# Kernel tuning notes

Measured on AMD Instinct MI355X. Metric: run time of the kernel, lower is better.

## Reference

```python
import jax, jax.numpy as jnp
import numpy as np

IN_DIM, INTER, OUT, CLS = 512, 128, 64, 4
MID, BOT = 1600, 6400
N = 1 + MID + BOT
E = 160000


def setup_inputs() -> dict:
    key = jax.random.key(0)
    ki = iter(jax.random.split(key, 48))

    def nrm(shape, s=0.02):
        return jax.random.normal(next(ki), shape, dtype=jnp.float32) * s

    z = lambda *s: jnp.zeros(s, jnp.float32)
    inp = {}
    inp["x"] = jax.random.normal(next(ki), (N, IN_DIM), dtype=jnp.float32)
    inp["edge_index"] = jax.random.randint(next(ki), (2, E), 0, N)
    # PatchRelevance 1 (in=512 -> 128)
    inp["Wq1"], inp["bq1"] = nrm((IN_DIM, INTER)), z(INTER)
    inp["Wk1"], inp["bk1"] = nrm((IN_DIM, INTER)), z(INTER)
    inp["Wv1"], inp["bv1"] = nrm((IN_DIM, INTER)), z(INTER)
    # PatchRelevance 2 (128 -> 64)
    inp["Wq2"], inp["bq2"] = nrm((INTER, OUT)), z(OUT)
    inp["Wk2"], inp["bk2"] = nrm((INTER, OUT)), z(OUT)
    inp["Wv2"], inp["bv2"] = nrm((INTER, OUT)), z(OUT)
    # GCN convs
    inp["Wg1"], inp["bg1"] = nrm((IN_DIM, INTER)), z(INTER)
    inp["Wg2"], inp["bg2"] = nrm((INTER, OUT)), z(OUT)
    # squeeze MLPs
    inp["Ws1"], inp["bs1"] = nrm((2 * INTER, INTER)), z(INTER)
    inp["Ws2"], inp["bs2"] = nrm((2 * OUT, OUT)), z(OUT)
    # heads
    inp["Wfc1"], inp["bfc1"] = nrm((3 * OUT, OUT)), z(OUT)
    inp["Wfc2"], inp["bfc2"] = nrm((OUT, CLS)), z(CLS)
    inp["Wtw"], inp["btw"] = nrm((OUT, CLS)), z(CLS)
    inp["Wmid"], inp["bmid"] = nrm((OUT, CLS)), z(CLS)
    inp["Wbot"], inp["bbot"] = nrm((OUT, CLS)), z(CLS)
    # sparse_attention Conv1d(out_dim -> 4, k=4, s=4)  weight layout OIH
    inp["Wconv"] = nrm((4, OUT, 4))
    inp["bconv"] = z(4)
    inp["arch0"] = MID
    inp["arch1"] = BOT
    return inp


def _patch_rel(x, Wq, bq, Wk, bk, Wv, bv):
    q = x @ Wq + bq
    k = x @ Wk + bk
    v = x @ Wv + bv
    att = jax.nn.softmax(q @ k.T, axis=-1)  # [N, N]
    return att @ v


def _gcn(x, src, dst, W, b, n):
    # PyG GCNConv: add self-loops (already in src/dst), symmetric deg^-1/2 norm
    deg = jax.ops.segment_sum(jnp.ones_like(src, dtype=x.dtype), dst, num_segments=n)
    dinv = jnp.where(deg > 0, jax.lax.rsqrt(deg), 0.0)
    norm = dinv[src] * dinv[dst]
    h = x @ W
    out = jax.ops.segment_sum(h[src] * norm[:, None], dst, num_segments=n)
    return out + b


def reference(x, edge_index, Wq1, bq1, Wk1, bk1, Wv1, bv1, Wq2, bq2, Wk2, bk2,
              Wv2, bv2, Wg1, bg1, Wg2, bg2, Ws1, bs1, Ws2, bs2, Wfc1, bfc1,
              Wfc2, bfc2, Wtw, btw, Wmid, bmid, Wbot, bbot, Wconv, bconv,
              arch0, arch1):
    n = x.shape[0]
    loop = jnp.arange(n, dtype=edge_index.dtype)
    src = jnp.concatenate([edge_index[0], loop])
    dst = jnp.concatenate([edge_index[1], loop])

    r1 = _patch_rel(x, Wq1, bq1, Wk1, bk1, Wv1, bv1)
    g1 = _gcn(x, src, dst, Wg1, bg1, n)
    s1 = jax.nn.relu(jax.nn.relu(jnp.concatenate([g1, r1], axis=1)) @ Ws1 + bs1)

    r2 = _patch_rel(s1, Wq2, bq2, Wk2, bk2, Wv2, bv2)
    g2 = _gcn(s1, src, dst, Wg2, bg2, n)
    s2 = jax.nn.relu(jax.nn.relu(jnp.concatenate([g2, r2], axis=1)) @ Ws2 + bs2)

    tw = s2[0:1]                                   # [1, OUT]
    mid_features = s2[1:1 + arch0]                 # [arch0, OUT]
    mid_avg = jnp.mean(mid_features, axis=0, keepdims=True)
    bf = s2[1 + arch0:1 + arch0 + arch1]           # [arch1, OUT]

    # Conv1d(OUT -> 4, k=4, s=4) over node axis: [1, OUT, arch1] -> [1, 4, arch0]
    bw = jax.lax.conv_general_dilated(bf.T[None], Wconv, (4,), 'VALID',
                                      dimension_numbers=('NCH', 'OIH', 'NCH'))[0]
    bw = bw + bconv[:, None]                       # [4, arch0]
    # index_copy_ with strided indices == interleave channels: wv[i*4+j] = bw[j, i]
    wv = bw.T.reshape(-1)
    wv = wv / jnp.max(wv)
    grp = wv.reshape(arch0, 4)
    grp = grp / jnp.sum(jnp.abs(grp), axis=-1, keepdims=True)
    wv = grp.reshape(arch1, 1)

    tree_bottom = ((wv * bf).T.reshape(-1, arch0, 4).sum(-1)).T  # [arch0, OUT]
    bottom_weighted = (jnp.sum(wv * bf, axis=0) / arch0).reshape(1, -1)

    out_tw = tw @ Wtw + btw
    out_mid = mid_avg @ Wmid + bmid
    out_bottom = bottom_weighted @ Wbot + bbot
    gcn_feat = jnp.concatenate([tw, mid_avg, bottom_weighted], axis=-1) @ Wfc1 + bfc1
    out_gcn = jax.nn.relu(gcn_feat) @ Wfc2 + bfc2
    return (out_gcn, out_tw, out_mid, out_bottom, gcn_feat, tw, mid_avg,
            bottom_weighted, wv, mid_features, tree_bottom)
```

## Files before the change

### kernel.cpp

```cpp
#include <hip/hip_runtime.h>
#include <math.h>

#define N_NODES 8001
#define NPAD    8032
#define E_EDGES 160000
#define NQTOT   8064
#define LOG2E   1.4426950408889634f
#define NSPLIT  16

typedef unsigned short u16;
typedef __attribute__((ext_vector_type(8)))  short bf16x8;
typedef __attribute__((ext_vector_type(16))) float f32x16;

__device__ __forceinline__ short f2bf(float f) {
    unsigned u = __builtin_bit_cast(unsigned, f);
    u = (u + 0x7FFFu + ((u >> 16) & 1u)) >> 16;
    return (short)u;
}
__device__ __forceinline__ float bf2f(u16 x) {
    return __builtin_bit_cast(float, (unsigned)x << 16);
}
__device__ __forceinline__ int pk2(float a, float b) {
    int r;
    asm("v_cvt_pk_bf16_f32 %0, %1, %2" : "=v"(r) : "v"(a), "v"(b));
    return r;
}

#define GLDS(g, l) __builtin_amdgcn_global_load_lds( \
    (const __attribute__((address_space(1))) void*)(g), \
    (__attribute__((address_space(3))) void*)(l), 16, 0, 0)

__global__ __launch_bounds__(256) void prep_all(
    const float* __restrict__ x, const int* __restrict__ ei,
    const float* __restrict__ Wq1, const float* __restrict__ Wk1,
    const float* __restrict__ Wv1, const float* __restrict__ Wg1,
    const float* __restrict__ Wq2, const float* __restrict__ Wk2,
    const float* __restrict__ Wv2, const float* __restrict__ Wg2,
    const float* __restrict__ Ws1, const float* __restrict__ Ws2,
    int* __restrict__ degi, u16* __restrict__ XB,
    u16* __restrict__ WT1, u16* __restrict__ WT2,
    u16* __restrict__ WST1, u16* __restrict__ WST2)
{
    const int b = blockIdx.x, tid = threadIdx.x;
    if (b < 625) {
        int e = b * 256 + tid;
        if (e < E_EDGES) atomicAdd(&degi[ei[E_EDGES + e]], 1);
    } else if (b < 2633) {
        size_t t = (size_t)(b - 625) * 256 + tid;
        int row = (int)(t / 64), c8 = (int)(t % 64) * 8;
        int lrow = min(row, N_NODES - 1);
        const float4* p = (const float4*)&x[(size_t)lrow * 512 + c8];
        float4 u = p[0], v = p[1];
        int4 w = { pk2(u.x, u.y), pk2(u.z, u.w), pk2(v.x, v.y), pk2(v.z, v.w) };
        *(int4*)&XB[t * 8] = w;
    } else if (b < 3657) {
        int t = (b - 2633) * 256 + tid;
        int p = t / (128 * 512), n = (t / 512) & 127, k = t % 512;
        const float* W = (p == 0) ? Wq1 : (p == 1) ? Wk1 : (p == 2) ? Wv1 : Wg1;
        float v = W[k * 128 + n];
        if (p == 0) v *= LOG2E;
        WT1[t] = (u16)f2bf(v);
    } else if (b < 3785) {
        int t = (b - 3657) * 256 + tid;
        int p = t / (64 * 128), n = (t / 128) & 63, k = t & 127;
        const float* W = (p == 0) ? Wq2 : (p == 1) ? Wk2 : (p == 2) ? Wv2 : Wg2;
        float v = W[k * 64 + n];
        if (p == 0) v *= LOG2E;
        WT2[t] = (u16)f2bf(v);
    } else if (b < 3913) {
        int t = (b - 3785) * 256 + tid;
        int n = t >> 8, k = t & 255;
        WST1[t] = (u16)f2bf(Ws1[k * 128 + n]);
    } else {
        int t = (b - 3913) * 256 + tid;
        int n = t >> 7, k = t & 127;
        WST2[t] = (u16)f2bf(Ws2[k * 64 + n]);
    }
}

template<int K, int MOUT>
__global__ __launch_bounds__(256) void proj4_mfma(
    const u16* __restrict__ Xb, const u16* __restrict__ WT,
    const float* __restrict__ bq, const float* __restrict__ bk,
    const float* __restrict__ bv,
    u16* __restrict__ Qb, u16* __restrict__ Kb, u16* __restrict__ VTb,
    float* __restrict__ Hb)
{
    constexpr int NKC  = K / 16;
    constexpr int NNT  = MOUT / 32;
    constexpr int ROWB = K / 8;
    constexpr int NB   = 32 * ROWB;

    __shared__ u16 xs[32 * K];

    const int tid = threadIdx.x, wid = tid >> 6, lane = tid & 63;
    const int q = lane & 31, gp = lane >> 5;
    const int m0 = blockIdx.x * 32;

    for (int i = tid; i < NB; i += 256) {
        int row = i / ROWB, blk = i % ROWB;
        GLDS(&Xb[(size_t)(m0 + row) * K + 8 * (blk ^ (row & 7))], &xs[i * 8]);
    }
    __syncthreads();

    f32x16 acc[NNT];
#pragma unroll
    for (int nt = 0; nt < NNT; nt++) acc[nt] = f32x16{};

    const u16* wbase = WT + (size_t)wid * MOUT * K;

#pragma unroll 4
    for (int c = 0; c < NKC; c++) {
        bf16x8 af = *(const bf16x8*)&xs[q * K + 8 * ((2 * c + gp) ^ (q & 7))];
#pragma unroll
        for (int nt = 0; nt < NNT; nt++) {
            bf16x8 bf = *(const bf16x8*)&wbase[(size_t)(nt * 32 + q) * K + 16 * c + 8 * gp];
            acc[nt] = __builtin_amdgcn_mfma_f32_32x32x16_bf16(af, bf, acc[nt], 0, 0, 0);
        }
    }

    if (wid == 0) {
#pragma unroll
        for (int nt = 0; nt < NNT; nt++) {
            float bb = bq[nt * 32 + q] * LOG2E;
#pragma unroll
            for (int r = 0; r < 16; r++) {
                int grow = m0 + (r & 3) + 8 * (r >> 2) + 4 * gp;
                Qb[(size_t)grow * MOUT + nt * 32 + q] = (u16)f2bf(acc[nt][r] + bb);
            }
        }
    } else if (wid == 1) {
#pragma unroll
        for (int nt = 0; nt < NNT; nt++) {
            float bb = bk[nt * 32 + q];
#pragma unroll
            for (int r = 0; r < 16; r++) {
                int grow = m0 + (r & 3) + 8 * (r >> 2) + 4 * gp;
                Kb[(size_t)grow * MOUT + nt * 32 + q] = (u16)f2bf(acc[nt][r] + bb);
            }
        }
    } else if (wid == 2) {
#pragma unroll
        for (int nt = 0; nt < NNT; nt++) {
            float bb = bv[nt * 32 + q];
            u16* vrow = &VTb[(size_t)(nt * 32 + q) * NPAD];
#pragma unroll
            for (int g = 0; g < 4; g++) {
                ushort4 s;
                s.x = (u16)f2bf(acc[nt][4 * g + 0] + bb);
                s.y = (u16)f2bf(acc[nt][4 * g + 1] + bb);
                s.z = (u16)f2bf(acc[nt][4 * g + 2] + bb);
                s.w = (u16)f2bf(acc[nt][4 * g + 3] + bb);
                *(ushort4*)&vrow[m0 + 8 * g + 4 * gp] = s;
            }
        }
    } else {
#pragma unroll
        for (int nt = 0; nt < NNT; nt++) {
#pragma unroll
            for (int r = 0; r < 16; r++) {
                int grow = m0 + (r & 3) + 8 * (r >> 2) + 4 * gp;
                if (grow < N_NODES)
                    Hb[(size_t)grow * MOUT + nt * 32 + q] = acc[nt][r];
            }
        }
    }
}

template<int K, int MOUT, int OM, int NW>
__global__ __launch_bounds__(NW * 64) void s_gemm_mfma(
    const u16* __restrict__ Ab, const u16* __restrict__ WT,
    const float* __restrict__ bias, void* __restrict__ Cv)
{
    constexpr int NKC  = K / 16;
    constexpr int ROWB = K / 8;
    constexpr int NB   = 32 * ROWB;

    __shared__ u16 xs[32 * K];

    const int tid = threadIdx.x, wid = tid >> 6, lane = tid & 63;
    const int q = lane & 31, gp = lane >> 5;
    const int m0 = blockIdx.x * 32;

    for (int i = tid; i < NB; i += NW * 64) {
        int row = i / ROWB, blk = i % ROWB;
        GLDS(&Ab[(size_t)(m0 + row) * K + 8 * (blk ^ (row & 7))], &xs[i * 8]);
    }
    __syncthreads();

    f32x16 acc = f32x16{};
    const u16* wbase = WT + (size_t)(wid * 32) * K;

#pragma unroll 4
    for (int c = 0; c < NKC; c++) {
        bf16x8 af = *(const bf16x8*)&xs[q * K + 8 * ((2 * c + gp) ^ (q & 7))];
        bf16x8 bf = *(const bf16x8*)&wbase[(size_t)q * K + 16 * c + 8 * gp];
        acc = __builtin_amdgcn_mfma_f32_32x32x16_bf16(af, bf, acc, 0, 0, 0);
    }

    float bb = bias[wid * 32 + q];
#pragma unroll
    for (int r = 0; r < 16; r++) {
        int grow = m0 + (r & 3) + 8 * (r >> 2) + 4 * gp;
        float v = fmaxf(acc[r] + bb, 0.f);
        if (OM == 0) {
            if (grow < N_NODES) ((float*)Cv)[(size_t)grow * MOUT + wid * 32 + q] = v;
        } else {
            ((u16*)Cv)[(size_t)grow * MOUT + wid * 32 + q] = (u16)f2bf(v);
        }
    }
}

template<int D, int S>
__global__ __launch_bounds__(256) void attn_split(
    const u16* __restrict__ Qg, const u16* __restrict__ Kg,
    const u16* __restrict__ VTg, u16* __restrict__ PO, float* __restrict__ PL)
{
    constexpr int NCH   = D / 16;
    constexpr int NDT   = D / 32;
    constexpr int KROWB = D / 8;
    constexpr int KI    = (32 * D) / 512;
    constexpr int VI    = (D * 32) / 512;
    constexpr int NKS   = KI / 4;
    constexpr int NVS   = VI / 4;
    constexpr int NT    = (N_NODES + 31) / 32;
    constexpr int CHUNK = (NT + S - 1) / S;

    __shared__ u16 kb[2][32 * D];
    __shared__ u16 vb[2][D * 32];

    const int tid  = threadIdx.x;
    const int wid  = tid >> 6;
    const int lane = tid & 63;
    const int q    = lane & 31;
    const int gp   = lane >> 5;
    const int sp   = blockIdx.x;
    const int q0   = blockIdx.y * 128 + wid * 32;

    bf16x8 qf[NCH];
    {
        int row = min(q0 + q, N_NODES - 1);
        const u16* qr = &Qg[(size_t)row * D + 8 * gp];
#pragma unroll
        for (int c = 0; c < NCH; c++)
            qf[c] = *(const bf16x8*)&qr[16 * c];
    }

    const int arow = (q & ~12) | ((q & 4) << 1) | ((q & 8) >> 1);
    const int hK   = (arow & 3) | (((arow >> 3) & 1) << 2);

    f32x16 acc[NDT];
#pragma unroll
    for (int i = 0; i < NDT; i++) acc[i] = f32x16{};
    float l = 0.f;

    const int t0 = sp * CHUNK;
    const int t1 = min(t0 + CHUNK, NT);

    const u16* kp[NKS]; int kdo[NKS];
#pragma unroll
    for (int s = 0; s < NKS; s++) {
        int i   = wid + 4 * s;
        int B   = i * 64 + lane;
        int row = B / KROWB;
        int bk  = B & (KROWB - 1);
        int h   = (row & 3) | (((row >> 3) & 1) << 2);
        kp[s]  = &Kg[(size_t)(t0 * 32 + row) * D + 8 * (bk ^ h)];
        kdo[s] = i * 512;
    }
    const u16* vp[NVS]; int vdo[NVS];
#pragma unroll
    for (int s = 0; s < NVS; s++) {
        int i  = wid + 4 * s;
        int B  = i * 64 + lane;
        int d  = B >> 2;
        int bv = B & 3;
        vp[s]  = &VTg[(size_t)d * NPAD + t0 * 32 + 8 * (bv ^ (d & 3))];
        vdo[s] = i * 512;
    }

    auto stage = [&](int buf) {
        u16* kdst = &kb[buf][0];
        u16* vdst = &vb[buf][0];
#pragma unroll
        for (int s = 0; s < NKS; s++) GLDS(kp[s], &kdst[kdo[s]]);
#pragma unroll
        for (int s = 0; s < NVS; s++) GLDS(vp[s], &vdst[vdo[s]]);
    };
    auto advance = [&]() {
#pragma unroll
        for (int s = 0; s < NKS; s++) kp[s] += 32 * D;
#pragma unroll
        for (int s = 0; s < NVS; s++) vp[s] += 32;
    };

    stage(0);
    advance();
    __syncthreads();

    for (int t = t0; t < t1; t++) {
        const int b = (t - t0) & 1;
        if (t + 1 < t1) { stage(b ^ 1); advance(); }

        const u16* kbt = &kb[b][0];
        const u16* vbt = &vb[b][0];
        const int j0 = t * 32;

        f32x16 st = f32x16{};
#pragma unroll
        for (int c = 0; c < NCH; c++) {
            bf16x8 af = *(const bf16x8*)&kbt[arow * D + 8 * ((2 * c + gp) ^ hK)];
            st = __builtin_amdgcn_mfma_f32_32x32x16_bf16(af, qf[c], st, 0, 0, 0);
        }

        if (j0 + 32 > N_NODES) {
#pragma unroll
            for (int r = 0; r < 16; r++) {
                int kl = (r & 3) + (((r >> 2) & 1) << 2) + ((r >> 3) << 4) + 8 * gp;
                if (j0 + kl >= N_NODES) st[r] = -INFINITY;
            }
        }

        float pv[16]; float ps = 0.f;
#pragma unroll
        for (int r = 0; r < 16; r++) { pv[r] = exp2f(st[r]); ps += pv[r]; }
        ps += __shfl_xor(ps, 32);
        l += ps;

        int4 w0 = { pk2(pv[0],  pv[1]),  pk2(pv[2],  pv[3]),
                    pk2(pv[4],  pv[5]),  pk2(pv[6],  pv[7]) };
        int4 w1 = { pk2(pv[8],  pv[9]),  pk2(pv[10], pv[11]),
                    pk2(pv[12], pv[13]), pk2(pv[14], pv[15]) };
        bf16x8 bp0 = __builtin_bit_cast(bf16x8, w0);
        bf16x8 bp1 = __builtin_bit_cast(bf16x8, w1);

#pragma unroll
        for (int dt = 0; dt < NDT; dt++) {
            const int d = 32 * dt + q;
            bf16x8 vf0 = *(const bf16x8*)&vbt[d * 32 + 8 * ((gp)     ^ (d & 3))];
            acc[dt] = __builtin_amdgcn_mfma_f32_32x32x16_bf16(vf0, bp0, acc[dt], 0, 0, 0);
            bf16x8 vf1 = *(const bf16x8*)&vbt[d * 32 + 8 * ((2 + gp) ^ (d & 3))];
            acc[dt] = __builtin_amdgcn_mfma_f32_32x32x16_bf16(vf1, bp1, acc[dt], 0, 0, 0);
        }
        __syncthreads();
    }

    const int qrl = q0 + q;
    if (gp == 0) PL[(size_t)sp * NQTOT + qrl] = l;
    u16* po = &PO[((size_t)sp * NQTOT + qrl) * D];
#pragma unroll
    for (int dt = 0; dt < NDT; dt++)
#pragma unroll
        for (int k = 0; k < 4; k++) {
            int2 w = { pk2(acc[dt][4 * k + 0], acc[dt][4 * k + 1]),
                       pk2(acc[dt][4 * k + 2], acc[dt][4 * k + 3]) };
            *(int2*)&po[32 * dt + 8 * k + 4 * gp] = w;
        }
}

template<int C, int S>
__global__ __launch_bounds__(256) void merge_gather(
    const u16* __restrict__ PO, const float* __restrict__ PL,
    const float* __restrict__ h, const int* __restrict__ rowptr,
    const int2* __restrict__ csr, const float* __restrict__ dinv,
    const float* __restrict__ bias, u16* __restrict__ AR)
{
    constexpr int MB  = (NPAD * (C / 4)) / 256;
    constexpr int LPN = C / 4;
    constexpr int NPB = 256 / LPN;

    const int tid = threadIdx.x;
    if ((int)blockIdx.x < MB) {
        int t  = blockIdx.x * 256 + tid;
        int qr = t / (C / 4);
        int d4 = (t % (C / 4)) * 4;

        float L = 0.f;
#pragma unroll
        for (int s = 0; s < S; s++) L += PL[(size_t)s * NQTOT + qr];
        float4 o = make_float4(0.f, 0.f, 0.f, 0.f);
#pragma unroll
        for (int s = 0; s < S; s++) {
            ushort4 p = *(const ushort4*)&PO[((size_t)s * NQTOT + qr) * C + d4];
            o.x += bf2f(p.x); o.y += bf2f(p.y);
            o.z += bf2f(p.z); o.w += bf2f(p.w);
        }
        float inv = 1.f / L;
        int2 w = { pk2(fmaxf(o.x * inv, 0.f), fmaxf(o.y * inv, 0.f)),
                   pk2(fmaxf(o.z * inv, 0.f), fmaxf(o.w * inv, 0.f)) };
        *(int2*)&AR[(size_t)qr * (2 * C) + C + d4] = w;
    } else {
        const int node = (blockIdx.x - MB) * NPB + tid / LPN;
        const int c4   = (tid % LPN) * 4;
        if (node >= N_NODES) return;
        const int r0 = rowptr[node], r1 = rowptr[node + 1];
        float4 acc = make_float4(0.f, 0.f, 0.f, 0.f);
        for (int j = r0; j < r1; j++) {
            int2 pk = csr[j];
            float nr = __int_as_float(pk.y);
            const float4 hv = *(const float4*)&h[(size_t)pk.x * C + c4];
            acc.x += hv.x * nr; acc.y += hv.y * nr;
            acc.z += hv.z * nr; acc.w += hv.w * nr;
        }
        float di = dinv[node];
        float sl = di * di;
        const float4 hs = *(const float4*)&h[(size_t)node * C + c4];
        const float4 bv = *(const float4*)&bias[c4];
        acc.x += hs.x * sl + bv.x; acc.y += hs.y * sl + bv.y;
        acc.z += hs.z * sl + bv.z; acc.w += hs.w * sl + bv.w;
        int2 w = { pk2(fmaxf(acc.x, 0.f), fmaxf(acc.y, 0.f)),
                   pk2(fmaxf(acc.z, 0.f), fmaxf(acc.w, 0.f)) };
        *(int2*)&AR[(size_t)node * (2 * C) + c4] = w;
    }
}

__global__ __launch_bounds__(256) void prefix_rowptr(
    const int* __restrict__ degi, int* __restrict__ rowptr,
    int* __restrict__ cursor, float* __restrict__ dinv)
{
    __shared__ int sums[256];
    const int t = threadIdx.x;
    const int base = t * 32;
    int local[32];
    int s = 0;
#pragma unroll
    for (int i = 0; i < 32; i++) {
        int idx = base + i;
        local[i] = s;
        s += (idx < N_NODES) ? degi[idx] : 0;
    }
    sums[t] = s;
    __syncthreads();
    for (int o = 1; o < 256; o <<= 1) {
        int v = (t >= o) ? sums[t - o] : 0;
        __syncthreads();
        sums[t] += v;
        __syncthreads();
    }
    const int pre = (t == 0) ? 0 : sums[t - 1];
#pragma unroll
    for (int i = 0; i < 32; i++) {
        int idx = base + i;
        if (idx <= N_NODES) {
            int v = pre + local[i];
            rowptr[idx] = v;
            if (idx < N_NODES) cursor[idx] = v;
        }
    }
    for (int i = t; i < N_NODES; i += 256)
        dinv[i] = rsqrtf((float)degi[i] + 1.f);
}

__global__ void csr_fill(const int* __restrict__ ei, const float* __restrict__ dinv,
                         int* __restrict__ cursor, int2* __restrict__ csr)
{
    int e = blockIdx.x * blockDim.x + threadIdx.x;
    if (e >= E_EDGES) return;
    int s = ei[e], d = ei[E_EDGES + e];
    int pos = atomicAdd(&cursor[d], 1);
    int2 pk;
    pk.x = s;
    pk.y = __float_as_int(dinv[s] * dinv[d]);
    csr[pos] = pk;
}

__global__ __launch_bounds__(256) void conv_wv(
    const float* __restrict__ S2, const float* __restrict__ Wconv,
    const float* __restrict__ bconv, float* __restrict__ wvp)
{
    __shared__ float wt[16 * 64];
    const int tid = threadIdx.x;
    for (int idx = tid; idx < 1024; idx += 256) {
        int o = idx >> 8, rem = idx & 255, i = rem >> 2, k = rem & 3;
        wt[(k * 4 + o) * 64 + i] = Wconv[idx];
    }
    __syncthreads();

    const int wid = tid >> 6, d = tid & 63;
    const int t = blockIdx.x * 4 + wid;
    const float* base = S2 + (size_t)(1601 + 4 * t) * 64;
    const float v0 = base[d], v1 = base[64 + d], v2 = base[128 + d], v3 = base[192 + d];

    float p[4];
#pragma unroll
    for (int o = 0; o < 4; o++)
        p[o] = v0 * wt[(0 * 4 + o) * 64 + d] + v1 * wt[(1 * 4 + o) * 64 + d]
             + v2 * wt[(2 * 4 + o) * 64 + d] + v3 * wt[(3 * 4 + o) * 64 + d];

#pragma unroll
    for (int o = 0; o < 4; o++)
#pragma unroll
        for (int off = 1; off < 64; off <<= 1) p[o] += __shfl_xor(p[o], off);

    if (d == 0) {
#pragma unroll
        for (int o = 0; o < 4; o++) wvp[4 * t + o] = p[o] + bconv[o];
    }
}

__global__ __launch_bounds__(256) void wv_copy(
    const float* __restrict__ wvp, const float* __restrict__ S2,
    float* __restrict__ wv, float* __restrict__ out)
{
    const int b = blockIdx.x, tid = threadIdx.x;
    if (b < 7) {
        float mv = -INFINITY;
        for (int i = tid; i < 6400; i += 256) mv = fmaxf(mv, wvp[i]);
#pragma unroll
        for (int o = 32; o > 0; o >>= 1) mv = fmaxf(mv, __shfl_xor(mv, o));
        __shared__ float sm[4];
        if ((tid & 63) == 0) sm[tid >> 6] = mv;
        __syncthreads();
        const float g = fmaxf(fmaxf(sm[0], sm[1]), fmaxf(sm[2], sm[3]));
        int t = b * 256 + tid;
        if (t < 1600) {
            float v0 = wvp[4 * t + 0] / g, v1 = wvp[4 * t + 1] / g;
            float v2 = wvp[4 * t + 2] / g, v3 = wvp[4 * t + 3] / g;
            float s = fabsf(v0) + fabsf(v1) + fabsf(v2) + fabsf(v3);
            float r0 = v0 / s, r1 = v1 / s, r2 = v2 / s, r3 = v3 / s;
            wv[4 * t + 0] = r0; wv[4 * t + 1] = r1;
            wv[4 * t + 2] = r2; wv[4 * t + 3] = r3;
            out[272 + 4 * t + 0] = r0; out[272 + 4 * t + 1] = r1;
            out[272 + 4 * t + 2] = r2; out[272 + 4 * t + 3] = r3;
        }
    } else {
        int i = (b - 7) * 256 + tid;
        if (i < 25600) ((float4*)(out + 6672))[i] = ((const float4*)(S2 + 64))[i];
    }
}

__global__ void tree_bottom_kernel(const float* __restrict__ S2,
                                   const float* __restrict__ wv,
                                   float* __restrict__ out)
{
    int t = blockIdx.x * blockDim.x + threadIdx.x;
    if (t >= 1600 * 64) return;
    int mg = t >> 6, c = t & 63;
    const float* base = S2 + (size_t)(1601 + 4 * mg) * 64 + c;
    out[t] = wv[4 * mg + 0] * base[0]   + wv[4 * mg + 1] * base[64]
           + wv[4 * mg + 2] * base[128] + wv[4 * mg + 3] * base[192];
}

__global__ void col_mean2(const float* __restrict__ S2, const float* __restrict__ tb,
                          float* __restrict__ midavg, float* __restrict__ botw)
{
    const int b = blockIdx.x;
    const int c = b & 63;
    const float* in = (b < 64) ? (S2 + 64) : tb;
    float s = 0.f;
    for (int r = threadIdx.x; r < 1600; r += 256) s += in[(size_t)r * 64 + c];
    for (int o = 32; o > 0; o >>= 1) s += __shfl_xor(s, o);
    __shared__ float sm[4];
    if ((threadIdx.x & 63) == 0) sm[threadIdx.x >> 6] = s;
    __syncthreads();
    if (threadIdx.x == 0) {
        float v = (sm[0] + sm[1] + sm[2] + sm[3]) * (1.f / 1600.f);
        (b < 64 ? midavg : botw)[c] = v;
    }
}

__global__ void head_kernel(const float* __restrict__ S2,
                            const float* __restrict__ midavg, const float* __restrict__ botw,
                            const float* __restrict__ Wtw,  const float* __restrict__ btw,
                            const float* __restrict__ Wmid, const float* __restrict__ bmid,
                            const float* __restrict__ Wbot, const float* __restrict__ bbot,
                            const float* __restrict__ Wfc1, const float* __restrict__ bfc1,
                            const float* __restrict__ Wfc2, const float* __restrict__ bfc2,
                            float* __restrict__ out)
{
    __shared__ float cat[192];
    __shared__ float gf[64];
    int t = threadIdx.x;
    float twv = S2[t];
    cat[t]       = twv;
    cat[64 + t]  = midavg[t];
    cat[128 + t] = botw[t];
    out[80 + t]  = twv;
    out[144 + t] = midavg[t];
    out[208 + t] = botw[t];
    __syncthreads();
    float acc = bfc1[t];
    for (int k = 0; k < 192; k++) acc += cat[k] * Wfc1[k * 64 + t];
    gf[t] = acc;
    out[16 + t] = acc;
    __syncthreads();
    if (t < 4) {
        float og = bfc2[t], ot = btw[t], om = bmid[t], ob = bbot[t];
        for (int c = 0; c < 64; c++) {
            og += fmaxf(gf[c], 0.f) * Wfc2[c * 4 + t];
            ot += cat[c]        * Wtw[c * 4 + t];
            om += cat[64 + c]   * Wmid[c * 4 + t];
            ob += cat[128 + c]  * Wbot[c * 4 + t];
        }
        out[0 + t] = og; out[4 + t] = ot; out[8 + t] = om; out[12 + t] = ob;
    }
}

extern "C" void kernel_launch(void* const* d_in, const int* in_sizes, int n_in,
                              void* d_out, int out_size, void* d_ws, size_t ws_size,
                              hipStream_t stream)
{
    (void)in_sizes; (void)n_in; (void)out_size; (void)ws_size;
    const float* x    = (const float*)d_in[0];
    const int*   ei   = (const int*)d_in[1];
    const float* Wq1  = (const float*)d_in[2];  const float* bq1 = (const float*)d_in[3];
    const float* Wk1  = (const float*)d_in[4];  const float* bk1 = (const float*)d_in[5];
    const float* Wv1  = (const float*)d_in[6];  const float* bv1 = (const float*)d_in[7];
    const float* Wq2  = (const float*)d_in[8];  const float* bq2 = (const float*)d_in[9];
    const float* Wk2  = (const float*)d_in[10]; const float* bk2 = (const float*)d_in[11];
    const float* Wv2  = (const float*)d_in[12]; const float* bv2 = (const float*)d_in[13];
    const float* Wg1  = (const float*)d_in[14]; const float* bg1 = (const float*)d_in[15];
    const float* Wg2  = (const float*)d_in[16]; const float* bg2 = (const float*)d_in[17];
    const float* Ws1  = (const float*)d_in[18]; const float* bs1 = (const float*)d_in[19];
    const float* Ws2  = (const float*)d_in[20]; const float* bs2 = (const float*)d_in[21];
    const float* Wfc1 = (const float*)d_in[22]; const float* bfc1= (const float*)d_in[23];
    const float* Wfc2 = (const float*)d_in[24]; const float* bfc2= (const float*)d_in[25];
    const float* Wtw  = (const float*)d_in[26]; const float* btw = (const float*)d_in[27];
    const float* Wmid = (const float*)d_in[28]; const float* bmid= (const float*)d_in[29];
    const float* Wbot = (const float*)d_in[30]; const float* bbot= (const float*)d_in[31];
    const float* Wconv= (const float*)d_in[32]; const float* bconv=(const float*)d_in[33];

    float* out = (float*)d_out;
    float* ws  = (float*)d_ws;

    const size_t N128 = (size_t)N_NODES * 128;
    const size_t BF128 = (size_t)NPAD * 128 / 2;

    size_t off = 0;
    auto alloc = [&](size_t n) { float* p = ws + off; off += (n + 15) & ~size_t(15); return p; };
    float* QB1  = alloc(BF128);
    float* KB1  = alloc(BF128);
    float* VTB1 = alloc(BF128);
    float* XB   = alloc((size_t)NPAD * 256);
    float* WT1  = alloc(4 * 128 * 512 / 2);
    float* WT2  = alloc(4 * 64 * 128 / 2);
    float* WST1 = alloc(128 * 256 / 2);
    float* WST2 = alloc(64 * 128 / 2);
    float* AR1  = alloc((size_t)NPAD * 128);
    float* S1B  = alloc((size_t)NPAD * 64);
    float* H1   = alloc(N128);
    float* S2   = alloc(N128);
    float* DINV = alloc(N_NODES);
    int*   DEGI   = (int*)alloc(8008);
    int*   ROWPTR = (int*)alloc(8008);
    int*   CURSOR = (int*)alloc(8008);
    int2*  CSR    = (int2*)alloc(2 * (size_t)E_EDGES);
    float* PO   = alloc((size_t)NSPLIT * NQTOT * 128 / 2);
    float* PL   = alloc((size_t)NSPLIT * NQTOT);
    float* WVP  = alloc(6400);
    float* WV   = alloc(6400);
    float* MIDAVG = alloc(64);
    float* BOTW   = alloc(64);
    float* QB2  = QB1;
    float* KB2  = KB1;
    float* VTB2 = VTB1;
    float* H2   = H1;
    float* AR2  = AR1;

    hipMemsetAsync(DEGI, 0, N_NODES * sizeof(int), stream);
    prep_all<<<3945, 256, 0, stream>>>(
        x, ei, Wq1, Wk1, Wv1, Wg1, Wq2, Wk2, Wv2, Wg2, Ws1, Ws2,
        DEGI, (u16*)XB, (u16*)WT1, (u16*)WT2, (u16*)WST1, (u16*)WST2);
    prefix_rowptr<<<1, 256, 0, stream>>>(DEGI, ROWPTR, CURSOR, DINV);
    csr_fill<<<(E_EDGES + 255) / 256, 256, 0, stream>>>(ei, DINV, CURSOR, CSR);

    proj4_mfma<512, 128><<<NPAD / 32, 256, 0, stream>>>(
        (const u16*)XB, (const u16*)WT1, bq1, bk1, bv1,
        (u16*)QB1, (u16*)KB1, (u16*)VTB1, H1);

    attn_split<128, NSPLIT><<<dim3(NSPLIT, 63), 256, 0, stream>>>(
        (const u16*)QB1, (const u16*)KB1, (const u16*)VTB1, (u16*)PO, PL);

    {
        int mb = (NPAD * 32) / 256, gb = (N_NODES * 32 + 255) / 256;
        merge_gather<128, NSPLIT><<<mb + gb, 256, 0, stream>>>(
            (const u16*)PO, PL, H1, ROWPTR, CSR, DINV, bg1, (u16*)AR1);
    }

    s_gemm_mfma<256, 128, 1, 4><<<NPAD / 32, 256, 0, stream>>>(
        (const u16*)AR1, (const u16*)WST1, bs1, (u16*)S1B);

    proj4_mfma<128, 64><<<NPAD / 32, 256, 0, stream>>>(
        (const u16*)S1B, (const u16*)WT2, bq2, bk2, bv2,
        (u16*)QB2, (u16*)KB2, (u16*)VTB2, H2);

    attn_split<64, NSPLIT><<<dim3(NSPLIT, 63), 256, 0, stream>>>(
        (const u16*)QB2, (const u16*)KB2, (const u16*)VTB2, (u16*)PO, PL);

    {
        int mb = (NPAD * 16) / 256, gb = (N_NODES * 16 + 255) / 256;
        merge_gather<64, NSPLIT><<<mb + gb, 256, 0, stream>>>(
            (const u16*)PO, PL, H2, ROWPTR, CSR, DINV, bg2, (u16*)AR2);
    }

    s_gemm_mfma<128, 64, 0, 2><<<NPAD / 32, 128, 0, stream>>>(
        (const u16*)AR2, (const u16*)WST2, bs2, S2);

    conv_wv<<<400, 256, 0, stream>>>(S2, Wconv, bconv, WVP);
    wv_copy<<<107, 256, 0, stream>>>(WVP, S2, WV, out);
    tree_bottom_kernel<<<400, 256, 0, stream>>>(S2, WV, out + 109072);
    col_mean2<<<128, 256, 0, stream>>>(S2, out + 109072, MIDAVG, BOTW);
    head_kernel<<<1, 64, 0, stream>>>(S2, MIDAVG, BOTW, Wtw, btw, Wmid, bmid,
                                      Wbot, bbot, Wfc1, bfc1, Wfc2, bfc2, out);
}
```

Before: 248.1 us.

## Raise MFMA priority, split layer-2 attention wider, fold column means into other kernels

Wraps the QK and PV MFMA loops in attn_split with s_setprio so matrix work gets scheduling priority over other waves. The second attention layer now uses 32 key splits instead of 16 to expose more parallelism for the smaller head dimension. The separate col_mean2 launch is removed: the mid-feature mean is computed by extra blocks of conv_wv, and the bottom-weighted mean is accumulated with atomics inside tree_bottom_kernel. This saves a launch and a reread of the tree_bottom output, at the cost of float atomics with nondeterministic summation order and a larger partial-output merge for layer 2.

```diff
diff --git a/kernel.cpp b/kernel.cpp
--- a/kernel.cpp
+++ b/kernel.cpp
@@ -6,7 +6,8 @@
 #define E_EDGES 160000
 #define NQTOT   8064
 #define LOG2E   1.4426950408889634f
-#define NSPLIT  16
+#define SP1     16
+#define SP2     32
 
 typedef unsigned short u16;
 typedef __attribute__((ext_vector_type(8)))  short bf16x8;
@@ -307,11 +308,13 @@
         const int j0 = t * 32;
 
         f32x16 st = f32x16{};
+        __builtin_amdgcn_s_setprio(1);
 #pragma unroll
         for (int c = 0; c < NCH; c++) {
             bf16x8 af = *(const bf16x8*)&kbt[arow * D + 8 * ((2 * c + gp) ^ hK)];
             st = __builtin_amdgcn_mfma_f32_32x32x16_bf16(af, qf[c], st, 0, 0, 0);
         }
+        __builtin_amdgcn_s_setprio(0);
 
         if (j0 + 32 > N_NODES) {
 #pragma unroll
@@ -334,6 +337,7 @@
         bf16x8 bp0 = __builtin_bit_cast(bf16x8, w0);
         bf16x8 bp1 = __builtin_bit_cast(bf16x8, w1);
 
+        __builtin_amdgcn_s_setprio(1);
 #pragma unroll
         for (int dt = 0; dt < NDT; dt++) {
             const int d = 32 * dt + q;
@@ -342,6 +346,7 @@
             bf16x8 vf1 = *(const bf16x8*)&vbt[d * 32 + 8 * ((2 + gp) ^ (d & 3))];
             acc[dt] = __builtin_amdgcn_mfma_f32_32x32x16_bf16(vf1, bp1, acc[dt], 0, 0, 0);
         }
+        __builtin_amdgcn_s_setprio(0);
         __syncthreads();
     }
 
@@ -466,35 +471,48 @@
 
 __global__ __launch_bounds__(256) void conv_wv(
     const float* __restrict__ S2, const float* __restrict__ Wconv,
-    const float* __restrict__ bconv, float* __restrict__ wvp)
-{
-    __shared__ float wt[16 * 64];
-    const int tid = threadIdx.x;
-    for (int idx = tid; idx < 1024; idx += 256) {
-        int o = idx >> 8, rem = idx & 255, i = rem >> 2, k = rem & 3;
-        wt[(k * 4 + o) * 64 + i] = Wconv[idx];
-    }
-    __syncthreads();
-
-    const int wid = tid >> 6, d = tid & 63;
-    const int t = blockIdx.x * 4 + wid;
-    const float* base = S2 + (size_t)(1601 + 4 * t) * 64;
-    const float v0 = base[d], v1 = base[64 + d], v2 = base[128 + d], v3 = base[192 + d];
-
-    float p[4];
-#pragma unroll
-    for (int o = 0; o < 4; o++)
-        p[o] = v0 * wt[(0 * 4 + o) * 64 + d] + v1 * wt[(1 * 4 + o) * 64 + d]
-             + v2 * wt[(2 * 4 + o) * 64 + d] + v3 * wt[(3 * 4 + o) * 64 + d];
-
-#pragma unroll
-    for (int o = 0; o < 4; o++)
-#pragma unroll
-        for (int off = 1; off < 64; off <<= 1) p[o] += __shfl_xor(p[o], off);
-
-    if (d == 0) {
-#pragma unroll
-        for (int o = 0; o < 4; o++) wvp[4 * t + o] = p[o] + bconv[o];
+    const float* __restrict__ bconv, float* __restrict__ wvp,
+    float* __restrict__ midavg)
+{
+    const int b = blockIdx.x, tid = threadIdx.x;
+    if (b < 400) {
+        __shared__ float wt[16 * 64];
+        for (int idx = tid; idx < 1024; idx += 256) {
+            int o = idx >> 8, rem = idx & 255, i = rem >> 2, k = rem & 3;
+            wt[(k * 4 + o) * 64 + i] = Wconv[idx];
+        }
+        __syncthreads();
+
+        const int wid = tid >> 6, d = tid & 63;
+        const int t = b * 4 + wid;
+        const float* base = S2 + (size_t)(1601 + 4 * t) * 64;
+        const float v0 = base[d], v1 = base[64 + d], v2 = base[128 + d], v3 = base[192 + d];
+
+        float p[4];
+#pragma unroll
+        for (int o = 0; o < 4; o++)
+            p[o] = v0 * wt[(0 * 4 + o) * 64 + d] + v1 * wt[(1 * 4 + o) * 64 + d]
+                 + v2 * wt[(2 * 4 + o) * 64 + d] + v3 * wt[(3 * 4 + o) * 64 + d];
+
+#pragma unroll
+        for (int o = 0; o < 4; o++)
+#pragma unroll
+            for (int off = 1; off < 64; off <<= 1) p[o] += __shfl_xor(p[o], off);
+
+        if (d == 0) {
+#pragma unroll
+            for (int o = 0; o < 4; o++) wvp[4 * t + o] = p[o] + bconv[o];
+        }
+    } else {
+        const int c = b - 400;
+        float s = 0.f;
+        for (int r = tid; r < 1600; r += 256) s += S2[64 + (size_t)r * 64 + c];
+        for (int o = 32; o > 0; o >>= 1) s += __shfl_xor(s, o);
+        __shared__ float sm[4];
+        if ((tid & 63) == 0) sm[tid >> 6] = s;
+        __syncthreads();
+        if (tid == 0)
+            midavg[c] = (sm[0] + sm[1] + sm[2] + sm[3]) * (1.f / 1600.f);
     }
 }
 
@@ -529,38 +547,28 @@
     }
 }
 
-__global__ void tree_bottom_kernel(const float* __restrict__ S2,
-                                   const float* __restrict__ wv,
-                                   float* __restrict__ out)
-{
-    int t = blockIdx.x * blockDim.x + threadIdx.x;
-    if (t >= 1600 * 64) return;
+__global__ __launch_bounds__(256) void tree_bottom_kernel(
+    const float* __restrict__ S2, const float* __restrict__ wv,
+    float* __restrict__ out, float* __restrict__ botw_raw)
+{
+    __shared__ float red[256];
+    int t = blockIdx.x * 256 + threadIdx.x;
     int mg = t >> 6, c = t & 63;
     const float* base = S2 + (size_t)(1601 + 4 * mg) * 64 + c;
-    out[t] = wv[4 * mg + 0] * base[0]   + wv[4 * mg + 1] * base[64]
-           + wv[4 * mg + 2] * base[128] + wv[4 * mg + 3] * base[192];
-}
-
-__global__ void col_mean2(const float* __restrict__ S2, const float* __restrict__ tb,
-                          float* __restrict__ midavg, float* __restrict__ botw)
-{
-    const int b = blockIdx.x;
-    const int c = b & 63;
-    const float* in = (b < 64) ? (S2 + 64) : tb;
-    float s = 0.f;
-    for (int r = threadIdx.x; r < 1600; r += 256) s += in[(size_t)r * 64 + c];
-    for (int o = 32; o > 0; o >>= 1) s += __shfl_xor(s, o);
-    __shared__ float sm[4];
-    if ((threadIdx.x & 63) == 0) sm[threadIdx.x >> 6] = s;
+    float v = wv[4 * mg + 0] * base[0]   + wv[4 * mg + 1] * base[64]
+            + wv[4 * mg + 2] * base[128] + wv[4 * mg + 3] * base[192];
+    out[t] = v;
+    red[threadIdx.x] = v;
     __syncthreads();
-    if (threadIdx.x == 0) {
-        float v = (sm[0] + sm[1] + sm[2] + sm[3]) * (1.f / 1600.f);
-        (b < 64 ? midavg : botw)[c] = v;
+    if (threadIdx.x < 64) {
+        float s = red[threadIdx.x] + red[threadIdx.x + 64]
+                + red[threadIdx.x + 128] + red[threadIdx.x + 192];
+        atomicAdd(&botw_raw[threadIdx.x], s);
     }
 }
 
 __global__ void head_kernel(const float* __restrict__ S2,
-                            const float* __restrict__ midavg, const float* __restrict__ botw,
+                            const float* __restrict__ midavg, const float* __restrict__ botw_raw,
                             const float* __restrict__ Wtw,  const float* __restrict__ btw,
                             const float* __restrict__ Wmid, const float* __restrict__ bmid,
                             const float* __restrict__ Wbot, const float* __restrict__ bbot,
@@ -572,12 +580,13 @@
     __shared__ float gf[64];
     int t = threadIdx.x;
     float twv = S2[t];
+    float bw  = botw_raw[t] * (1.f / 1600.f);
     cat[t]       = twv;
     cat[64 + t]  = midavg[t];
-    cat[128 + t] = botw[t];
+    cat[128 + t] = bw;
     out[80 + t]  = twv;
     out[144 + t] = midavg[t];
-    out[208 + t] = botw[t];
+    out[208 + t] = bw;
     __syncthreads();
     float acc = bfc1[t];
     for (int k = 0; k < 192; k++) acc += cat[k] * Wfc1[k * 64 + t];
@@ -645,8 +654,8 @@
     int*   ROWPTR = (int*)alloc(8008);
     int*   CURSOR = (int*)alloc(8008);
     int2*  CSR    = (int2*)alloc(2 * (size_t)E_EDGES);
-    float* PO   = alloc((size_t)NSPLIT * NQTOT * 128 / 2);
-    float* PL   = alloc((size_t)NSPLIT * NQTOT);
+    float* PO   = alloc((size_t)SP1 * NQTOT * 128 / 2);
+    float* PL   = alloc((size_t)SP2 * NQTOT);
     float* WVP  = alloc(6400);
     float* WV   = alloc(6400);
     float* MIDAVG = alloc(64);
@@ -658,6 +667,7 @@
     float* AR2  = AR1;
 
     hipMemsetAsync(DEGI, 0, N_NODES * sizeof(int), stream);
+    hipMemsetAsync(BOTW, 0, 64 * sizeof(float), stream);
     prep_all<<<3945, 256, 0, stream>>>(
         x, ei, Wq1, Wk1, Wv1, Wg1, Wq2, Wk2, Wv2, Wg2, Ws1, Ws2,
         DEGI, (u16*)XB, (u16*)WT1, (u16*)WT2, (u16*)WST1, (u16*)WST2);
@@ -668,12 +678,12 @@
         (const u16*)XB, (const u16*)WT1, bq1, bk1, bv1,
         (u16*)QB1, (u16*)KB1, (u16*)VTB1, H1);
 
-    attn_split<128, NSPLIT><<<dim3(NSPLIT, 63), 256, 0, stream>>>(
+    attn_split<128, SP1><<<dim3(SP1, 63), 256, 0, stream>>>(
         (const u16*)QB1, (const u16*)KB1, (const u16*)VTB1, (u16*)PO, PL);
 
     {
         int mb = (NPAD * 32) / 256, gb = (N_NODES * 32 + 255) / 256;
-        merge_gather<128, NSPLIT><<<mb + gb, 256, 0, stream>>>(
+        merge_gather<128, SP1><<<mb + gb, 256, 0, stream>>>(
             (const u16*)PO, PL, H1, ROWPTR, CSR, DINV, bg1, (u16*)AR1);
     }
 
@@ -684,22 +694,21 @@
         (const u16*)S1B, (const u16*)WT2, bq2, bk2, bv2,
         (u16*)QB2, (u16*)KB2, (u16*)VTB2, H2);
 
-    attn_split<64, NSPLIT><<<dim3(NSPLIT, 63), 256, 0, stream>>>(
+    attn_split<64, SP2><<<dim3(SP2, 63), 256, 0, stream>>>(
         (const u16*)QB2, (const u16*)KB2, (const u16*)VTB2, (u16*)PO, PL);
 
     {
         int mb = (NPAD * 16) / 256, gb = (N_NODES * 16 + 255) / 256;
-        merge_gather<64, NSPLIT><<<mb + gb, 256, 0, stream>>>(
+        merge_gather<64, SP2><<<mb + gb, 256, 0, stream>>>(
             (const u16*)PO, PL, H2, ROWPTR, CSR, DINV, bg2, (u16*)AR2);
     }
 
     s_gemm_mfma<128, 64, 0, 2><<<NPAD / 32, 128, 0, stream>>>(
         (const u16*)AR2, (const u16*)WST2, bs2, S2);
 
-    conv_wv<<<400, 256, 0, stream>>>(S2, Wconv, bconv, WVP);
+    conv_wv<<<464, 256, 0, stream>>>(S2, Wconv, bconv, WVP, MIDAVG);
     wv_copy<<<107, 256, 0, stream>>>(WVP, S2, WV, out);
-    tree_bottom_kernel<<<400, 256, 0, stream>>>(S2, WV, out + 109072);
-    col_mean2<<<128, 256, 0, stream>>>(S2, out + 109072, MIDAVG, BOTW);
+    tree_bottom_kernel<<<400, 256, 0, stream>>>(S2, WV, out + 109072, BOTW);
     head_kernel<<<1, 64, 0, stream>>>(S2, MIDAVG, BOTW, Wtw, btw, Wmid, bmid,
                                       Wbot, bbot, Wfc1, bfc1, Wfc2, bfc2, out);
 }
```

Measured after the change: 260.5 us. +5.0%, slower.
